# Kernel optimization log

Measured on AMD Instinct MI355X. Metric: run time of the kernel, lower is better.

The kernel has to match this reference:

```python
import jax, jax.numpy as jnp
import numpy as np


def setup_inputs() -> dict:
    key = jax.random.key(0)
    inp = jax.random.normal(key, (8, 3, 224, 224), dtype=jnp.float32)
    return {"inp": inp, "tau_min": 1, "tau_max": 60, "ntau": 8,
            "num_angles": 12, "stride": 2}


def _logpolar_offsets(tau_min, tau_max, ntau, num_angles):
    # Matches the torch module: theta in [-pi, pi), tau logarithmically spaced,
    # coords stacked angle-major as (y, x) pairs (theta unsqueeze(1) outer).
    c = (tau_max / tau_min) ** (1.0 / (ntau - 1)) - 1.0
    theta = np.arange(num_angles, dtype=np.float64) * (2.0 * np.pi / num_angles) - np.pi
    tau = tau_min * (1.0 + c) ** np.arange(ntau, dtype=np.float64)
    x = tau[None, :] * np.cos(theta[:, None])   # (A, T)
    y = tau[None, :] * np.sin(theta[:, None])   # (A, T)
    return (jnp.asarray(y.ravel(), jnp.float32),
            jnp.asarray(x.ravel(), jnp.float32))  # each (A*T,)


def reference(inp, tau_min, tau_max, ntau, num_angles, stride):
    yoff, xoff = _logpolar_offsets(tau_min, tau_max, ntau, num_angles)
    B, F, H, W = inp.shape
    Hs = (H - 1) // stride + 1
    Ws = (W - 1) // stride + 1
    gy = jnp.arange(Hs, dtype=jnp.float32) * stride   # focus-point rows
    gx = jnp.arange(Ws, dtype=jnp.float32) * stride   # focus-point cols

    def sample(yo, xo):
        # Bilinear sample of inp at (i*stride + yo, j*stride + xo), zero outside.
        yq = gy + yo
        xq = gx + xo
        y0 = jnp.floor(yq)
        x0 = jnp.floor(xq)
        wy = (yq - y0)  # (Hs,)
        wx = (xq - x0)  # (Ws,)
        y0i = y0.astype(jnp.int32)
        x0i = x0.astype(jnp.int32)

        def gather(yi, xi):
            vy = ((yi >= 0) & (yi < H)).astype(inp.dtype)
            vx = ((xi >= 0) & (xi < W)).astype(inp.dtype)
            g = inp[:, :, jnp.clip(yi, 0, H - 1), :][:, :, :, jnp.clip(xi, 0, W - 1)]
            return g * (vy[:, None] * vx[None, :])  # (B,F,Hs,Ws)

        w00 = (1 - wy)[:, None] * (1 - wx)[None, :]
        w01 = (1 - wy)[:, None] * wx[None, :]
        w10 = wy[:, None] * (1 - wx)[None, :]
        w11 = wy[:, None] * wx[None, :]
        return (w00 * gather(y0i, x0i) + w01 * gather(y0i, x0i + 1)
                + w10 * gather(y0i + 1, x0i) + w11 * gather(y0i + 1, x0i + 1))

    out = jax.vmap(sample)(yoff, xoff)                    # (A*T, B, F, Hs, Ws)
    out = out.reshape(num_angles, ntau, B, F, Hs, Ws)
    out = jnp.transpose(out, (2, 3, 1, 0, 4, 5))          # (B, F, ntau, A, Hs, Ws)
    return out
```

## Files before the change

kernel.cpp:

```cpp
#include <hip/hip_runtime.h>
#include <cmath>
#include <algorithm>

#ifndef M_PI
#define M_PI 3.14159265358979323846
#endif

#define B_ 8
#define F_ 3
#define H_ 224
#define W_ 224
#define T_ 8
#define A_ 12
#define NK 96
#define STRIDE_ 2
#define HS_ 112
#define WS_ 112
#define PLANE_ (H_ * W_)
#define SLICE_ (HS_ * WS_)

#define RI 8
#define BANDROWS 78
#define PITCH 225
#define HALF 112

struct LPArgs {
    int   cy[NK];  int cx[NK];
    float fy[NK];  float fx[NK];
    int   korig[NK];
    int   cymin[2]; int cymax[2];
};

static LPArgs make_args() {
    int cy[NK], cx[NK]; float fy[NK], fx[NK];
    double c = pow(60.0, 1.0 / 7.0) - 1.0;
    for (int t = 0; t < T_; ++t) {
        double tau = pow(1.0 + c, (double)t);
        for (int a = 0; a < A_; ++a) {
            double th = (double)a * (2.0 * M_PI / (double)A_) - M_PI;
            float yo = (float)(tau * sin(th)), xo = (float)(tau * cos(th));
            int k = t * A_ + a;
            float yf = floorf(yo), xf = floorf(xo);
            cy[k] = (int)yf; fy[k] = yo - yf;
            cx[k] = (int)xf; fx[k] = xo - xf;
        }
    }
    int idx[NK];
    for (int k = 0; k < NK; ++k) idx[k] = k;
    std::sort(idx, idx + NK, [&](int a, int b) { return cy[a] < cy[b]; });
    LPArgs r;
    r.cymin[0] = r.cymin[1] = 1000; r.cymax[0] = r.cymax[1] = -1000;
    for (int p = 0; p < NK; ++p) {
        int k = idx[p], g = p / 48;
        r.cy[p] = cy[k]; r.cx[p] = cx[k];
        r.fy[p] = fy[k]; r.fx[p] = fx[k];
        r.korig[p] = k;
        r.cymin[g] = std::min(r.cymin[g], cy[k]);
        r.cymax[g] = std::max(r.cymax[g], cy[k]);
    }
    return r;
}

__global__ __launch_bounds__(1024, 8) void lp_sample_kernel(
    const float* __restrict__ inp, float* __restrict__ out, LPArgs args) {

    __shared__ float lds[BANDROWS * PITCH];

    const int bf = blockIdx.x;
    const int i0 = blockIdx.y * RI;
    const int g  = blockIdx.z;

    const int r0 = max(0, 2 * i0 + args.cymin[g]);
    const int r1 = min(H_ - 1, 2 * i0 + 2 * (RI - 1) + args.cymax[g] + 1);
    const int nrows = min(r1 - r0 + 1, BANDROWS);

    const float* plane = inp + (size_t)bf * PLANE_;

    {
        const int n = nrows * (W_ / 4);
        for (int v = threadIdx.x; v < n; v += 1024) {
            const unsigned r = (unsigned)v / 56u;
            const int u = v - (int)r * 56;
            const float4 val = *(const float4*)(plane + (size_t)(r0 + (int)r) * W_ + 4 * u);
            float* rowp = lds + r * PITCH;
            const int e = 2 * u;
            rowp[e]            = val.x;
            rowp[e + 1]        = val.z;
            rowp[HALF + e]     = val.y;
            rowp[HALF + e + 1] = val.w;
        }
    }
    __syncthreads();

    const int lane = threadIdx.x & 63;
    const int wave = __builtin_amdgcn_readfirstlane(threadIdx.x >> 6);

    float* outp = out + (size_t)bf * (NK * SLICE_) + (size_t)i0 * WS_;

#pragma unroll 1
    for (int tt = 0; tt < 6; ++tt) {
        const int task = wave + (tt << 4);
        const int kl   = task >> 1;
        const int h    = task & 1;
        const int kk   = g * 48 + kl;

        const int   cy = args.cy[kk]; const float fy = args.fy[kk];
        const int   cx = args.cx[kk]; const float fx = args.fx[kk];
        const int   ko = args.korig[kk];
        const int   P  = cx & 1;

        const int j   = h * 64 + lane;
        const int ix0 = 2 * j + cx;
        const float wLv = (ix0 >= 0  && ix0 <= W_ - 1) ? (1.0f - fx) : 0.0f;
        const float wRv = (ix0 >= -1 && ix0 <= W_ - 2) ? fx          : 0.0f;
        int eidx = (ix0 + P) >> 1;
        int oidx = (ix0 + 1 - P) >> 1;
        eidx = min(max(eidx, 0), HALF - 1);
        oidx = min(max(oidx, 0), HALF - 1);
        const float wE = P ? wRv : wLv;
        const float wO = P ? wLv : wRv;

        const float* eptr = lds + eidx;
        const float* optr = lds + HALF + oidx;

        float* orow = outp + (size_t)ko * SLICE_ + j;

        if (j < WS_) {
#pragma unroll 2
            for (int di = 0; di < RI; ++di) {
                const int iy0 = 2 * (i0 + di) + cy;
                float mA, mB;
                if (iy0 >= 0 && iy0 <= H_ - 2)  { mA = 1.0f - fy; mB = fy; }
                else if (iy0 == -1)             { mA = fy;        mB = 0.0f; }
                else if (iy0 == H_ - 1)         { mA = 0.0f;      mB = 1.0f - fy; }
                else                            { mA = 0.0f;      mB = 0.0f; }
                const int by = min(max(iy0, 0), H_ - 2);
                const int rb = (by - r0) * PITCH;

                const float e0 = eptr[rb], e1 = eptr[rb + PITCH];
                const float o0 = optr[rb], o1 = optr[rb + PITCH];

                const float rr = wE * (mA * e0 + mB * e1)
                               + wO * (mA * o0 + mB * o1);

                orow[(size_t)di * WS_] = rr;
            }
        }
    }
}

extern "C" void kernel_launch(void* const* d_in, const int* in_sizes, int n_in,
                              void* d_out, int out_size, void* d_ws, size_t ws_size,
                              hipStream_t stream) {
    const float* inp = (const float*)d_in[0];
    float*       out = (float*)d_out;

    static const LPArgs args = make_args();

    dim3 grid(B_ * F_, HS_ / RI, 2);
    lp_sample_kernel<<<grid, 1024, 0, stream>>>(inp, out, args);
}
```

Baseline: 133.3 us.

## Retile work into 8-offset groups with taller row bands and swizzled 1D grid

Splits the 96 log-polar offsets into 12 groups of 8 (sorted by vertical offset). Each block now covers 28 output rows in one pass, and each wave handles a single offset instead of looping over six tasks. The launch becomes a 1D grid with a block-index swizzle that spreads batch/channel planes across XCDs, and the LDS pitch changes to 224 with a row clamp. The taller, narrower bands cut redundant halo loading per output and make per-wave work uniform. In exchange, each group now reloads overlapping input bands, and an LDS pitch of 224 may bring back bank conflicts.

```diff
diff --git a/kernel.cpp b/kernel.cpp
--- a/kernel.cpp
+++ b/kernel.cpp
@@ -13,22 +13,24 @@
 #define T_ 8
 #define A_ 12
 #define NK 96
-#define STRIDE_ 2
 #define HS_ 112
 #define WS_ 112
 #define PLANE_ (H_ * W_)
 #define SLICE_ (HS_ * WS_)
 
-#define RI 8
-#define BANDROWS 78
-#define PITCH 225
+#define KG 8
+#define NG 12
+#define RI 28
+#define NIQ 4
+#define BANDROWS 91
+#define PITCH 224
 #define HALF 112
 
 struct LPArgs {
     int   cy[NK];  int cx[NK];
     float fy[NK];  float fx[NK];
     int   korig[NK];
-    int   cymin[2]; int cymax[2];
+    int   gmin[NG]; int gmax[NG];
 };
 
 static LPArgs make_args() {
@@ -49,14 +51,14 @@
     for (int k = 0; k < NK; ++k) idx[k] = k;
     std::sort(idx, idx + NK, [&](int a, int b) { return cy[a] < cy[b]; });
     LPArgs r;
-    r.cymin[0] = r.cymin[1] = 1000; r.cymax[0] = r.cymax[1] = -1000;
+    for (int g = 0; g < NG; ++g) { r.gmin[g] = 1000; r.gmax[g] = -1000; }
     for (int p = 0; p < NK; ++p) {
-        int k = idx[p], g = p / 48;
+        int k = idx[p], g = p / KG;
         r.cy[p] = cy[k]; r.cx[p] = cx[k];
         r.fy[p] = fy[k]; r.fx[p] = fx[k];
         r.korig[p] = k;
-        r.cymin[g] = std::min(r.cymin[g], cy[k]);
-        r.cymax[g] = std::max(r.cymax[g], cy[k]);
+        r.gmin[g] = std::min(r.gmin[g], cy[k]);
+        r.gmax[g] = std::max(r.gmax[g], cy[k]);
     }
     return r;
 }
@@ -66,12 +68,16 @@
 
     __shared__ float lds[BANDROWS * PITCH];
 
-    const int bf = blockIdx.x;
-    const int i0 = blockIdx.y * RI;
-    const int g  = blockIdx.z;
+    const int blk = (int)blockIdx.x;
+    const int swz = (blk & 7) * 144 + (blk >> 3);
+    const int bf  = swz / 48;
+    const int rem = swz - bf * 48;
+    const int kg  = rem >> 2;
+    const int iq  = rem & 3;
+    const int i0  = iq * RI;
 
-    const int r0 = max(0, 2 * i0 + args.cymin[g]);
-    const int r1 = min(H_ - 1, 2 * i0 + 2 * (RI - 1) + args.cymax[g] + 1);
+    const int r0 = max(0, 2 * i0 + args.gmin[kg]);
+    const int r1 = min(H_ - 1, 2 * i0 + 2 * (RI - 1) + args.gmax[kg] + 1);
     const int nrows = min(r1 - r0 + 1, BANDROWS);
 
     const float* plane = inp + (size_t)bf * PLANE_;
@@ -93,58 +99,52 @@
     __syncthreads();
 
     const int lane = threadIdx.x & 63;
-    const int wave = __builtin_amdgcn_readfirstlane(threadIdx.x >> 6);
+    const int wave = __builtin_amdgcn_readfirstlane((int)threadIdx.x >> 6);
 
-    float* outp = out + (size_t)bf * (NK * SLICE_) + (size_t)i0 * WS_;
+    const int kk = kg * KG + (wave >> 1);
+    const int h  = wave & 1;
 
-#pragma unroll 1
-    for (int tt = 0; tt < 6; ++tt) {
-        const int task = wave + (tt << 4);
-        const int kl   = task >> 1;
-        const int h    = task & 1;
-        const int kk   = g * 48 + kl;
+    const int   cy = args.cy[kk]; const float fy = args.fy[kk];
+    const int   cx = args.cx[kk]; const float fx = args.fx[kk];
+    const int   ko = args.korig[kk];
+    const int   P  = cx & 1;
 
-        const int   cy = args.cy[kk]; const float fy = args.fy[kk];
-        const int   cx = args.cx[kk]; const float fx = args.fx[kk];
-        const int   ko = args.korig[kk];
-        const int   P  = cx & 1;
+    const int j   = h * 64 + lane;
+    const int ix0 = 2 * j + cx;
+    const float wLv = (ix0 >= 0  && ix0 <= W_ - 1) ? (1.0f - fx) : 0.0f;
+    const float wRv = (ix0 >= -1 && ix0 <= W_ - 2) ? fx          : 0.0f;
+    int eidx = (ix0 + P) >> 1;
+    int oidx = (ix0 + 1 - P) >> 1;
+    eidx = min(max(eidx, 0), HALF - 1);
+    oidx = min(max(oidx, 0), HALF - 1);
+    const float wE = P ? wRv : wLv;
+    const float wO = P ? wLv : wRv;
 
-        const int j   = h * 64 + lane;
-        const int ix0 = 2 * j + cx;
-        const float wLv = (ix0 >= 0  && ix0 <= W_ - 1) ? (1.0f - fx) : 0.0f;
-        const float wRv = (ix0 >= -1 && ix0 <= W_ - 2) ? fx          : 0.0f;
-        int eidx = (ix0 + P) >> 1;
-        int oidx = (ix0 + 1 - P) >> 1;
-        eidx = min(max(eidx, 0), HALF - 1);
-        oidx = min(max(oidx, 0), HALF - 1);
-        const float wE = P ? wRv : wLv;
-        const float wO = P ? wLv : wRv;
+    const float* eptr = lds + eidx;
+    const float* optr = lds + HALF + oidx;
 
-        const float* eptr = lds + eidx;
-        const float* optr = lds + HALF + oidx;
+    float* orow = out + (size_t)bf * (NK * SLICE_) + (size_t)ko * SLICE_
+                      + (size_t)i0 * WS_ + j;
 
-        float* orow = outp + (size_t)ko * SLICE_ + j;
+    if (j < WS_) {
+#pragma unroll 4
+        for (int di = 0; di < RI; ++di) {
+            const int iy0 = 2 * (i0 + di) + cy;
+            float mA, mB;
+            if (iy0 >= 0 && iy0 <= H_ - 2)  { mA = 1.0f - fy; mB = fy; }
+            else if (iy0 == -1)             { mA = fy;        mB = 0.0f; }
+            else if (iy0 == H_ - 1)         { mA = 0.0f;      mB = 1.0f - fy; }
+            else                            { mA = 0.0f;      mB = 0.0f; }
+            const int by = min(max(iy0, 0), H_ - 2);
+            const int rb = min(by - r0, BANDROWS - 2) * PITCH;
 
-        if (j < WS_) {
-#pragma unroll 2
-            for (int di = 0; di < RI; ++di) {
-                const int iy0 = 2 * (i0 + di) + cy;
-                float mA, mB;
-                if (iy0 >= 0 && iy0 <= H_ - 2)  { mA = 1.0f - fy; mB = fy; }
-                else if (iy0 == -1)             { mA = fy;        mB = 0.0f; }
-                else if (iy0 == H_ - 1)         { mA = 0.0f;      mB = 1.0f - fy; }
-                else                            { mA = 0.0f;      mB = 0.0f; }
-                const int by = min(max(iy0, 0), H_ - 2);
-                const int rb = (by - r0) * PITCH;
+            const float e0 = eptr[rb], e1 = eptr[rb + PITCH];
+            const float o0 = optr[rb], o1 = optr[rb + PITCH];
 
-                const float e0 = eptr[rb], e1 = eptr[rb + PITCH];
-                const float o0 = optr[rb], o1 = optr[rb + PITCH];
+            const float rr = wE * (mA * e0 + mB * e1)
+                           + wO * (mA * o0 + mB * o1);
 
-                const float rr = wE * (mA * e0 + mB * e1)
-                               + wO * (mA * o0 + mB * o1);
-
-                orow[(size_t)di * WS_] = rr;
-            }
+            orow[(size_t)di * WS_] = rr;
         }
     }
 }
@@ -157,6 +157,5 @@
 
     static const LPArgs args = make_args();
 
-    dim3 grid(B_ * F_, HS_ / RI, 2);
-    lp_sample_kernel<<<grid, 1024, 0, stream>>>(inp, out, args);
+    lp_sample_kernel<<<dim3(24 * NG * NIQ), 1024, 0, stream>>>(inp, out, args);
 }
```

Measured after the change: 138.5 us. 3.9% more time.

## Use 4-phase LDS layout so each lane computes two outputs with float2 stores

Applied to the files above, without the earlier changes.

The LDS staging now splits each row into four phase-interleaved sub-rows instead of even/odd halves. Each lane produces two adjacent output columns and writes them as a float2, so one wave of 56 active lanes covers a whole output row. The tap loop shrinks from six half-row tasks to three full-row tasks per wave. The aim is fewer tasks, wider global stores and simpler index math, at the cost of eight LDS reads per row pair per lane and 8 of 64 lanes sitting idle.

```diff
diff --git a/kernel.cpp b/kernel.cpp
--- a/kernel.cpp
+++ b/kernel.cpp
@@ -13,7 +13,6 @@
 #define T_ 8
 #define A_ 12
 #define NK 96
-#define STRIDE_ 2
 #define HS_ 112
 #define WS_ 112
 #define PLANE_ (H_ * W_)
@@ -21,8 +20,9 @@
 
 #define RI 8
 #define BANDROWS 78
-#define PITCH 225
-#define HALF 112
+#define PH 57
+#define PITCH 228
+#define NLANE 56
 
 struct LPArgs {
     int   cy[NK];  int cx[NK];
@@ -82,50 +82,48 @@
             const unsigned r = (unsigned)v / 56u;
             const int u = v - (int)r * 56;
             const float4 val = *(const float4*)(plane + (size_t)(r0 + (int)r) * W_ + 4 * u);
-            float* rowp = lds + r * PITCH;
-            const int e = 2 * u;
-            rowp[e]            = val.x;
-            rowp[e + 1]        = val.z;
-            rowp[HALF + e]     = val.y;
-            rowp[HALF + e + 1] = val.w;
+            float* rowp = lds + r * PITCH + u;
+            rowp[0 * PH] = val.x;
+            rowp[1 * PH] = val.y;
+            rowp[2 * PH] = val.z;
+            rowp[3 * PH] = val.w;
         }
     }
     __syncthreads();
 
     const int lane = threadIdx.x & 63;
-    const int wave = __builtin_amdgcn_readfirstlane(threadIdx.x >> 6);
+    const int wave = __builtin_amdgcn_readfirstlane((int)threadIdx.x >> 6);
 
     float* outp = out + (size_t)bf * (NK * SLICE_) + (size_t)i0 * WS_;
+    const bool act = (lane < NLANE);
 
 #pragma unroll 1
-    for (int tt = 0; tt < 6; ++tt) {
-        const int task = wave + (tt << 4);
-        const int kl   = task >> 1;
-        const int h    = task & 1;
-        const int kk   = g * 48 + kl;
+    for (int tt = 0; tt < 3; ++tt) {
+        const int kk = g * 48 + wave + (tt << 4);
 
         const int   cy = args.cy[kk]; const float fy = args.fy[kk];
         const int   cx = args.cx[kk]; const float fx = args.fx[kk];
         const int   ko = args.korig[kk];
-        const int   P  = cx & 1;
+        const float omfx = 1.0f - fx;
 
-        const int j   = h * 64 + lane;
-        const int ix0 = 2 * j + cx;
-        const float wLv = (ix0 >= 0  && ix0 <= W_ - 1) ? (1.0f - fx) : 0.0f;
-        const float wRv = (ix0 >= -1 && ix0 <= W_ - 2) ? fx          : 0.0f;
-        int eidx = (ix0 + P) >> 1;
-        int oidx = (ix0 + 1 - P) >> 1;
-        eidx = min(max(eidx, 0), HALF - 1);
-        oidx = min(max(oidx, 0), HALF - 1);
-        const float wE = P ? wRv : wLv;
-        const float wO = P ? wLv : wRv;
+        const int l = lane;
+        const float* tp[4];
+        float tw[4];
+#pragma unroll
+        for (int t = 0; t < 4; ++t) {
+            const int s   = cx + t;
+            const int ct  = 4 * l + s;
+            const int ph  = s & 3;
+            int idx = l + (s >> 2);
+            idx = min(max(idx, 0), NLANE - 1);
+            tp[t] = lds + ph * PH + idx;
+            const float wbase = (t & 1) ? fx : omfx;
+            tw[t] = (ct >= 0 && ct < W_) ? wbase : 0.0f;
+        }
 
-        const float* eptr = lds + eidx;
-        const float* optr = lds + HALF + oidx;
+        float2* orow = (float2*)(outp + (size_t)ko * SLICE_) + l;
 
-        float* orow = outp + (size_t)ko * SLICE_ + j;
-
-        if (j < WS_) {
+        if (act) {
 #pragma unroll 2
             for (int di = 0; di < RI; ++di) {
                 const int iy0 = 2 * (i0 + di) + cy;
@@ -135,15 +133,20 @@
                 else if (iy0 == H_ - 1)         { mA = 0.0f;      mB = 1.0f - fy; }
                 else                            { mA = 0.0f;      mB = 0.0f; }
                 const int by = min(max(iy0, 0), H_ - 2);
-                const int rb = (by - r0) * PITCH;
+                const int rb = min(by - r0, BANDROWS - 2) * PITCH;
 
-                const float e0 = eptr[rb], e1 = eptr[rb + PITCH];
-                const float o0 = optr[rb], o1 = optr[rb + PITCH];
+                const float a0 = tp[0][rb], a1 = tp[0][rb + PITCH];
+                const float b0 = tp[1][rb], b1 = tp[1][rb + PITCH];
+                const float c0 = tp[2][rb], c1 = tp[2][rb + PITCH];
+                const float d0 = tp[3][rb], d1 = tp[3][rb + PITCH];
 
-                const float rr = wE * (mA * e0 + mB * e1)
-                               + wO * (mA * o0 + mB * o1);
+                float2 rr;
+                rr.x = mA * (tw[0] * a0 + tw[1] * b0)
+                     + mB * (tw[0] * a1 + tw[1] * b1);
+                rr.y = mA * (tw[2] * c0 + tw[3] * d0)
+                     + mB * (tw[2] * c1 + tw[3] * d1);
 
-                orow[(size_t)di * WS_] = rr;
+                orow[(size_t)di * (WS_ / 2)] = rr;
             }
         }
     }
@@ -157,6 +160,5 @@
 
     static const LPArgs args = make_args();
 
-    dim3 grid(B_ * F_, HS_ / RI, 2);
-    lp_sample_kernel<<<grid, 1024, 0, stream>>>(inp, out, args);
+    lp_sample_kernel<<<dim3(B_ * F_, HS_ / RI, 2), 1024, 0, stream>>>(inp, out, args);
 }
```

New measurement: 133.9 us. No clear change (+0.5%).
